# Kernel optimization log

Hardware: AMD Instinct MI355X
Metric: run time of the kernel (lower is better)

## Reference

```python
import jax, jax.numpy as jnp
import numpy as np

HEADS = 8
C_HEAD = 64  # head dim == in_dim of x
P0, P1 = 2, 3  # adaptive pool output


def setup_inputs() -> dict:
    key = jax.random.key(0)
    ks = jax.random.split(key, 8)
    b, c, h, w = 16, 64, 64, 96
    m, d = 6, 192
    inner = HEADS * C_HEAD  # 512
    return {
        "x": jax.random.normal(ks[0], (b, c, h, w), dtype=jnp.float32),
        "z": jax.random.normal(ks[1], (b, m, d), dtype=jnp.float32),
        "conv_w": jax.random.normal(ks[2], (192, c), dtype=jnp.float32) * 0.02,
        "conv_b": jax.random.normal(ks[3], (192,), dtype=jnp.float32) * 0.02,
        "wq": jax.random.normal(ks[4], (d, inner), dtype=jnp.float32) * 0.02,
        "bq": jax.random.normal(ks[5], (inner,), dtype=jnp.float32) * 0.02,
        "wo": jax.random.normal(ks[6], (inner, d), dtype=jnp.float32) * 0.02,
        "bo": jax.random.normal(ks[7], (d,), dtype=jnp.float32) * 0.02,
    }


def reference(x, z, conv_w, conv_b, wq, bq, wo, bo):
    b, c, h, w = x.shape
    _, m, d = z.shape
    # 1x1 conv (pointwise GEMM over channels) + bias
    xp = jnp.einsum('bchw,oc->bohw', x, conv_w) + conv_b[None, :, None, None]
    # AdaptiveAvgPool2d((2,3)) with exact divisibility -> block mean
    xp = xp.reshape(b, 192, P0, h // P0, P1, w // P1).mean(axis=(3, 5))  # [b,192,2,3]
    # view(b, d, m) then permute(0,2,1) -> [b, m, d]
    z = z + xp.reshape(b, d, m).transpose(0, 2, 1)
    # k = v: view(b, h*w, c), repeat heads along last dim, view(b, heads, h*w, c)
    # (row-major reshape reproduces torch .view semantics exactly)
    kv = jnp.tile(x.reshape(b, h * w, c), (1, 1, HEADS)).reshape(b, HEADS, h * w, C_HEAD)
    # q = Linear(dim, heads*c) then view(b, heads, m, c)
    q = (z @ wq + bq).reshape(b, HEADS, m, C_HEAD)
    scale = C_HEAD ** -0.5
    dots = jnp.einsum('bhmc,bhlc->bhml', q, kv) * scale  # [b,h,m,l]
    attn = jax.nn.softmax(dots, axis=-1)
    out = jnp.einsum('bhml,bhlc->bhmc', attn, kv)
    out = out.transpose(0, 2, 1, 3).reshape(b, m, HEADS * C_HEAD)  # b m (h c)
    return z + out @ wo + bo
```

## Files before the change

kernel.cpp:

```cpp
#include <hip/hip_runtime.h>

#define NB 16
#define NC 64
#define NM 6
#define ND 192
#define NHEADS 8
#define NCH 64
#define NINNER 512
#define PLANE 6144
#define XB (NC*PLANE)
#define NKEY 768
#define NCHUNK 8
#define CK 96

__global__ __launch_bounds__(256) void pool_kernel(const float* __restrict__ x,
                                                   float* __restrict__ xmean) {
    int bc = blockIdx.x;
    const float4* p = (const float4*)(x + (size_t)bc * PLANE);
    int tid = threadIdx.x;
    float acc[6] = {0.f,0.f,0.f,0.f,0.f,0.f};
    #pragma unroll
    for (int k = 0; k < 6; ++k) {
        int idx4 = tid + k * 256;
        int hh = idx4 / 24;
        int w4 = idx4 - hh * 24;
        int j = (hh >> 5) * 3 + (w4 >> 3);
        float4 v = p[idx4];
        acc[j] += v.x + v.y + v.z + v.w;
    }
    int lane = tid & 63, wave = tid >> 6;
    #pragma unroll
    for (int j = 0; j < 6; ++j) {
        float v = acc[j];
        for (int off = 32; off > 0; off >>= 1) v += __shfl_down(v, off, 64);
        acc[j] = v;
    }
    __shared__ float part[4][6];
    if (lane == 0) {
        #pragma unroll
        for (int j = 0; j < 6; ++j) part[wave][j] = acc[j];
    }
    __syncthreads();
    if (tid < 6) {
        float s = part[0][tid] + part[1][tid] + part[2][tid] + part[3][tid];
        xmean[bc * 6 + tid] = s * (1.0f / 1024.0f);
    }
}

__global__ __launch_bounds__(256) void zq_kernel(const float* __restrict__ z,
                                                 const float* __restrict__ conv_w,
                                                 const float* __restrict__ conv_b,
                                                 const float* __restrict__ wq,
                                                 const float* __restrict__ bq,
                                                 const float* __restrict__ xmean,
                                                 float* __restrict__ znew,
                                                 float* __restrict__ qr) {
    int blk = blockIdx.x;
    int cgrp = blk & 7, bm = blk >> 3;
    int b = bm / NM, m = bm - b * NM;
    int tid = threadIdx.x;
    __shared__ float xm[NC];
    __shared__ float zn[ND];
    __shared__ float qpart[3][64];
    if (tid < NC) xm[tid] = xmean[(b * NC + tid) * NM + m];
    __syncthreads();
    if (tid < ND) {
        float a = conv_b[tid];
        const float* wr = conv_w + tid * NC;
        #pragma unroll 16
        for (int c = 0; c < NC; ++c) a += wr[c] * xm[c];
        float v = z[bm * ND + tid] + a;
        zn[tid] = v;
        if (cgrp == 0) znew[bm * ND + tid] = v;
    }
    __syncthreads();
    int colL = tid & 63, ks = tid >> 6;
    int col = cgrp * 64 + colL;
    float a = (ks == 0) ? bq[col] : 0.f;
    int d0 = ks * 48;
    #pragma unroll 8
    for (int d = d0; d < d0 + 48; ++d) a += zn[d] * wq[d * NINNER + col];
    if (ks > 0) qpart[ks - 1][colL] = a;
    __syncthreads();
    if (ks == 0) {
        float tot = a + qpart[0][colL] + qpart[1][colL] + qpart[2][colL];
        int t = m * 8 + cgrp;
        qr[b * (48 * 64) + t * 64 + colL] = tot;
    }
}

__global__ __launch_bounds__(256, 4) void fattn_kernel(const float* __restrict__ x,
                                                       const float* __restrict__ qr,
                                                       float* __restrict__ po,
                                                       float* __restrict__ ps) {
    int blk = blockIdx.x;
    int chunk = blk & 7, bh = blk >> 3;
    int head = bh & 7, b = bh >> 3;
    int tid = threadIdx.x;
    __shared__ float k_lds[CK][NCH + 1];
    __shared__ float q_lds[NM][NCH];
    __shared__ float s_lds[NM][CK];
    __shared__ float pvp[3][NM][NCH];
    __shared__ float den_lds[NM];
    const float* kbase = x + (size_t)b * XB + (size_t)(head * NKEY + chunk * CK) * NCH;

    for (int i = tid; i < NM * NCH; i += 256) {
        int mi = i >> 6, ch = i & 63;
        q_lds[mi][ch] = qr[b * (48 * 64) + (head * NM + mi) * 64 + ch];
    }
    const float4* k4 = (const float4*)kbase;
    for (int i = tid; i < CK * 16; i += 256) {
        int row = i >> 4, c4 = i & 15;
        float4 v = k4[i];
        k_lds[row][c4 * 4 + 0] = v.x;
        k_lds[row][c4 * 4 + 1] = v.y;
        k_lds[row][c4 * 4 + 2] = v.z;
        k_lds[row][c4 * 4 + 3] = v.w;
    }
    __syncthreads();

    if (tid < 192) {
        int mip = (tid & 1) * 3, u = tid >> 1;
        float a0 = 0.f, a1 = 0.f, a2 = 0.f;
        #pragma unroll
        for (int c = 0; c < NCH; ++c) {
            float kv = k_lds[u][c];
            a0 += kv * q_lds[mip + 0][c];
            a1 += kv * q_lds[mip + 1][c];
            a2 += kv * q_lds[mip + 2][c];
        }
        s_lds[mip + 0][u] = __expf(a0 * 0.125f);
        s_lds[mip + 1][u] = __expf(a1 * 0.125f);
        s_lds[mip + 2][u] = __expf(a2 * 0.125f);
    }
    __syncthreads();

    int lane = tid & 63, wave = tid >> 6;
    #pragma unroll
    for (int rb = 0; rb < 2; ++rb) {
        int mi = rb * 4 + wave;
        if (mi < NM) {
            float v = s_lds[mi][lane] + ((lane < 32) ? s_lds[mi][64 + lane] : 0.f);
            for (int msk = 1; msk < 64; msk <<= 1) v += __shfl_xor(v, msk, 64);
            if (lane == 0) den_lds[mi] = v;
        }
    }

    float acc[NM] = {0.f,0.f,0.f,0.f,0.f,0.f};
    {
        int uq = tid >> 6, ch = tid & 63;
        int u0 = uq * 24;
        #pragma unroll 8
        for (int uu = u0; uu < u0 + 24; ++uu) {
            float kv = k_lds[uu][ch];
            #pragma unroll
            for (int mo = 0; mo < NM; ++mo) acc[mo] += s_lds[mo][uu] * kv;
        }
        if (uq > 0) {
            #pragma unroll
            for (int mo = 0; mo < NM; ++mo) pvp[uq - 1][mo][ch] = acc[mo];
        }
    }
    __syncthreads();
    if (tid < 64) {
        int ch = tid;
        #pragma unroll
        for (int mo = 0; mo < NM; ++mo) {
            float o = acc[mo] + pvp[0][mo][ch] + pvp[1][mo][ch] + pvp[2][mo][ch];
            po[(size_t)blk * (NM * NCH) + mo * NCH + ch] = o;
        }
    } else if (tid < 64 + NM) {
        ps[blk * NM + (tid - 64)] = den_lds[tid - 64];
    }
}

__global__ __launch_bounds__(256) void proj_kernel(const float* __restrict__ znew,
                                                   const float* __restrict__ po,
                                                   const float* __restrict__ ps,
                                                   const float* __restrict__ wo,
                                                   const float* __restrict__ bo,
                                                   float* __restrict__ out) {
    int blk = blockIdx.x;
    int cgrp = blk & 3, bm = blk >> 2;
    int b = bm / NM, m = bm - b * NM;
    int tid = threadIdx.x;
    __shared__ float orow[NINNER];
    __shared__ float part[3][48];

    for (int i = tid; i < NINNER; i += 256) {
        int h = i >> 6, ch = i & 63;
        int base = (b * NHEADS + h) * NCHUNK;
        float num = 0.f, den = 0.f;
        #pragma unroll
        for (int c = 0; c < NCHUNK; ++c) {
            num += po[(size_t)(base + c) * (NM * NCH) + m * NCH + ch];
            den += ps[(base + c) * NM + m];
        }
        orow[i] = num / den;
    }
    __syncthreads();

    int ks = tid / 48;
    int colL = tid - ks * 48;
    float a = 0.f;
    int col = cgrp * 48 + ((tid < 192) ? colL : 0);
    if (tid < 192) {
        int i0 = ks * 128;
        #pragma unroll 8
        for (int i = i0; i < i0 + 128; ++i) a += orow[i] * wo[i * ND + col];
        if (ks > 0) part[ks - 1][colL] = a;
    }
    __syncthreads();
    if (tid < 48) {
        float tot = a + part[0][colL] + part[1][colL] + part[2][colL]
                  + bo[col] + znew[bm * ND + col];
        out[bm * ND + col] = tot;
    }
}

extern "C" void kernel_launch(void* const* d_in, const int* in_sizes, int n_in,
                              void* d_out, int out_size, void* d_ws, size_t ws_size,
                              hipStream_t stream) {
    const float* x      = (const float*)d_in[0];
    const float* z      = (const float*)d_in[1];
    const float* conv_w = (const float*)d_in[2];
    const float* conv_b = (const float*)d_in[3];
    const float* wq     = (const float*)d_in[4];
    const float* bq     = (const float*)d_in[5];
    const float* wo     = (const float*)d_in[6];
    const float* bo     = (const float*)d_in[7];
    float* out = (float*)d_out;

    float* ws    = (float*)d_ws;
    float* xmean = ws;
    float* znew  = ws + 6144;
    float* qr    = ws + 24576;
    float* po    = ws + 73728;
    float* ps    = ws + 466944;

    pool_kernel<<<NB*NC, 256, 0, stream>>>(x, xmean);
    zq_kernel<<<NB*NM*8, 256, 0, stream>>>(z, conv_w, conv_b, wq, bq, xmean, znew, qr);
    fattn_kernel<<<NB*NHEADS*NCHUNK, 256, 0, stream>>>(x, qr, po, ps);
    proj_kernel<<<NB*NM*4, 256, 0, stream>>>(znew, po, ps, wo, bo, out);
}
```

Baseline: 37.04 us.

## Fuse z-update and q projection into attention kernel, prefetch K into registers

Removes the separate zq kernel by having each attention block recompute the updated z rows for its batch and the q vectors for its head, then run the chunked attention. K tiles are loaded into registers before the q computation to overlap global loads with that work, and shared memory is reused through a scratch buffer. This removes one launch and the qr workspace round trip, at the cost of heavily redundant per-block recomputation of z and q.

```diff
diff --git a/kernel.cpp b/kernel.cpp
--- a/kernel.cpp
+++ b/kernel.cpp
@@ -8,8 +8,6 @@
 #define NCH 64
 #define NINNER 512
 #define PLANE 6144
-#define XB (NC*PLANE)
-#define NKEY 768
 #define NCHUNK 8
 #define CK 96
 
@@ -47,91 +45,88 @@
     }
 }
 
-__global__ __launch_bounds__(256) void zq_kernel(const float* __restrict__ z,
-                                                 const float* __restrict__ conv_w,
-                                                 const float* __restrict__ conv_b,
-                                                 const float* __restrict__ wq,
-                                                 const float* __restrict__ bq,
-                                                 const float* __restrict__ xmean,
-                                                 float* __restrict__ znew,
-                                                 float* __restrict__ qr) {
+__global__ __launch_bounds__(256, 4) void qattn_kernel(
+    const float* __restrict__ x, const float* __restrict__ z,
+    const float* __restrict__ conv_w, const float* __restrict__ conv_b,
+    const float* __restrict__ wq, const float* __restrict__ bq,
+    const float* __restrict__ xmean,
+    float* __restrict__ znew, float* __restrict__ po, float* __restrict__ ps)
+{
     int blk = blockIdx.x;
-    int cgrp = blk & 7, bm = blk >> 3;
-    int b = bm / NM, m = bm - b * NM;
+    int b = blk >> 6, c = blk & 63;
+    int head = c >> 3;
     int tid = threadIdx.x;
-    __shared__ float xm[NC];
-    __shared__ float zn[ND];
-    __shared__ float qpart[3][64];
-    if (tid < NC) xm[tid] = xmean[(b * NC + tid) * NM + m];
-    __syncthreads();
-    if (tid < ND) {
-        float a = conv_b[tid];
-        const float* wr = conv_w + tid * NC;
-        #pragma unroll 16
-        for (int c = 0; c < NC; ++c) a += wr[c] * xm[c];
-        float v = z[bm * ND + tid] + a;
-        zn[tid] = v;
-        if (cgrp == 0) znew[bm * ND + tid] = v;
-    }
-    __syncthreads();
-    int colL = tid & 63, ks = tid >> 6;
-    int col = cgrp * 64 + colL;
-    float a = (ks == 0) ? bq[col] : 0.f;
-    int d0 = ks * 48;
-    #pragma unroll 8
-    for (int d = d0; d < d0 + 48; ++d) a += zn[d] * wq[d * NINNER + col];
-    if (ks > 0) qpart[ks - 1][colL] = a;
-    __syncthreads();
-    if (ks == 0) {
-        float tot = a + qpart[0][colL] + qpart[1][colL] + qpart[2][colL];
-        int t = m * 8 + cgrp;
-        qr[b * (48 * 64) + t * 64 + colL] = tot;
-    }
-}
-
-__global__ __launch_bounds__(256, 4) void fattn_kernel(const float* __restrict__ x,
-                                                       const float* __restrict__ qr,
-                                                       float* __restrict__ po,
-                                                       float* __restrict__ ps) {
-    int blk = blockIdx.x;
-    int chunk = blk & 7, bh = blk >> 3;
-    int head = bh & 7, b = bh >> 3;
-    int tid = threadIdx.x;
+
     __shared__ float k_lds[CK][NCH + 1];
     __shared__ float q_lds[NM][NCH];
-    __shared__ float s_lds[NM][CK];
-    __shared__ float pvp[3][NM][NCH];
-    __shared__ float den_lds[NM];
-    const float* kbase = x + (size_t)b * XB + (size_t)(head * NKEY + chunk * CK) * NCH;
-
-    for (int i = tid; i < NM * NCH; i += 256) {
-        int mi = i >> 6, ch = i & 63;
-        q_lds[mi][ch] = qr[b * (48 * 64) + (head * NM + mi) * 64 + ch];
-    }
-    const float4* k4 = (const float4*)kbase;
-    for (int i = tid; i < CK * 16; i += 256) {
-        int row = i >> 4, c4 = i & 15;
-        float4 v = k4[i];
-        k_lds[row][c4 * 4 + 0] = v.x;
-        k_lds[row][c4 * 4 + 1] = v.y;
-        k_lds[row][c4 * 4 + 2] = v.z;
-        k_lds[row][c4 * 4 + 3] = v.w;
-    }
-    __syncthreads();
+    __shared__ float scratch[1740];
+
+    float4 kreg[6];
+    {
+        const float4* k4 = (const float4*)(x + (size_t)blk * PLANE);
+        #pragma unroll
+        for (int r = 0; r < 6; ++r) kreg[r] = k4[tid + r * 256];
+    }
+
+    float* zn_s = scratch;
+    float* xm_s = scratch + 1152;
+    for (int i = tid; i < NC * NM; i += 256) xm_s[i] = xmean[b * (NC * NM) + i];
+    __syncthreads();
+
+    for (int i = tid; i < NM * ND; i += 256) {
+        int m = i / ND, d = i - m * ND;
+        float a = conv_b[d];
+        const float* wr = conv_w + d * NC;
+        #pragma unroll 16
+        for (int cc = 0; cc < NC; ++cc) a += wr[cc] * xm_s[cc * NM + m];
+        a += z[b * (NM * ND) + i];
+        zn_s[i] = a;
+        if (c == 0) znew[b * (NM * ND) + i] = a;
+    }
+    __syncthreads();
+
+    {
+        for (int idx = tid; idx < NM * NCH; idx += 256) {
+            int mi = idx >> 6, ch = idx & 63;
+            int flat = head * (NM * NCH) + idx;
+            int mrow = flat >> 9;
+            int col  = flat & 511;
+            float a = bq[col];
+            const float* zr = zn_s + mrow * ND;
+            #pragma unroll 8
+            for (int d = 0; d < ND; ++d) a += zr[d] * wq[d * NINNER + col];
+            q_lds[mi][ch] = a;
+        }
+    }
+
+    #pragma unroll
+    for (int r = 0; r < 6; ++r) {
+        int idx4 = tid + r * 256;
+        int u = idx4 >> 4, c4 = idx4 & 15;
+        k_lds[u][c4 * 4 + 0] = kreg[r].x;
+        k_lds[u][c4 * 4 + 1] = kreg[r].y;
+        k_lds[u][c4 * 4 + 2] = kreg[r].z;
+        k_lds[u][c4 * 4 + 3] = kreg[r].w;
+    }
+    __syncthreads();
+
+    float* s_s   = scratch;
+    float* pvp   = scratch + 576;
+    float* den_s = scratch + 1728;
 
     if (tid < 192) {
         int mip = (tid & 1) * 3, u = tid >> 1;
         float a0 = 0.f, a1 = 0.f, a2 = 0.f;
         #pragma unroll
-        for (int c = 0; c < NCH; ++c) {
-            float kv = k_lds[u][c];
-            a0 += kv * q_lds[mip + 0][c];
-            a1 += kv * q_lds[mip + 1][c];
-            a2 += kv * q_lds[mip + 2][c];
-        }
-        s_lds[mip + 0][u] = __expf(a0 * 0.125f);
-        s_lds[mip + 1][u] = __expf(a1 * 0.125f);
-        s_lds[mip + 2][u] = __expf(a2 * 0.125f);
+        for (int cc = 0; cc < NCH; ++cc) {
+            float kv = k_lds[u][cc];
+            a0 += kv * q_lds[mip + 0][cc];
+            a1 += kv * q_lds[mip + 1][cc];
+            a2 += kv * q_lds[mip + 2][cc];
+        }
+        s_s[(mip + 0) * CK + u] = __expf(a0 * 0.125f);
+        s_s[(mip + 1) * CK + u] = __expf(a1 * 0.125f);
+        s_s[(mip + 2) * CK + u] = __expf(a2 * 0.125f);
     }
     __syncthreads();
 
@@ -140,9 +135,9 @@
     for (int rb = 0; rb < 2; ++rb) {
         int mi = rb * 4 + wave;
         if (mi < NM) {
-            float v = s_lds[mi][lane] + ((lane < 32) ? s_lds[mi][64 + lane] : 0.f);
+            float v = s_s[mi * CK + lane] + ((lane < 32) ? s_s[mi * CK + 64 + lane] : 0.f);
             for (int msk = 1; msk < 64; msk <<= 1) v += __shfl_xor(v, msk, 64);
-            if (lane == 0) den_lds[mi] = v;
+            if (lane == 0) den_s[mi] = v;
         }
     }
 
@@ -154,11 +149,11 @@
         for (int uu = u0; uu < u0 + 24; ++uu) {
             float kv = k_lds[uu][ch];
             #pragma unroll
-            for (int mo = 0; mo < NM; ++mo) acc[mo] += s_lds[mo][uu] * kv;
+            for (int mo = 0; mo < NM; ++mo) acc[mo] += s_s[mo * CK + uu] * kv;
         }
         if (uq > 0) {
             #pragma unroll
-            for (int mo = 0; mo < NM; ++mo) pvp[uq - 1][mo][ch] = acc[mo];
+            for (int mo = 0; mo < NM; ++mo) pvp[((uq - 1) * NM + mo) * NCH + ch] = acc[mo];
         }
     }
     __syncthreads();
@@ -166,11 +161,13 @@
         int ch = tid;
         #pragma unroll
         for (int mo = 0; mo < NM; ++mo) {
-            float o = acc[mo] + pvp[0][mo][ch] + pvp[1][mo][ch] + pvp[2][mo][ch];
+            float o = acc[mo] + pvp[(0 * NM + mo) * NCH + ch]
+                              + pvp[(1 * NM + mo) * NCH + ch]
+                              + pvp[(2 * NM + mo) * NCH + ch];
             po[(size_t)blk * (NM * NCH) + mo * NCH + ch] = o;
         }
     } else if (tid < 64 + NM) {
-        ps[blk * NM + (tid - 64)] = den_lds[tid - 64];
+        ps[blk * NM + (tid - 64)] = den_s[tid - 64];
     }
 }
 
@@ -192,9 +189,9 @@
         int base = (b * NHEADS + h) * NCHUNK;
         float num = 0.f, den = 0.f;
         #pragma unroll
-        for (int c = 0; c < NCHUNK; ++c) {
-            num += po[(size_t)(base + c) * (NM * NCH) + m * NCH + ch];
-            den += ps[(base + c) * NM + m];
+        for (int cu = 0; cu < NCHUNK; ++cu) {
+            num += po[(size_t)(base + cu) * (NM * NCH) + m * NCH + ch];
+            den += ps[(base + cu) * NM + m];
         }
         orow[i] = num / den;
     }
@@ -234,12 +231,11 @@
     float* ws    = (float*)d_ws;
     float* xmean = ws;
     float* znew  = ws + 6144;
-    float* qr    = ws + 24576;
-    float* po    = ws + 73728;
-    float* ps    = ws + 466944;
+    float* po    = ws + 24576;
+    float* ps    = ws + 417792;
 
     pool_kernel<<<NB*NC, 256, 0, stream>>>(x, xmean);
-    zq_kernel<<<NB*NM*8, 256, 0, stream>>>(z, conv_w, conv_b, wq, bq, xmean, znew, qr);
-    fattn_kernel<<<NB*NHEADS*NCHUNK, 256, 0, stream>>>(x, qr, po, ps);
+    qattn_kernel<<<NB*NC, 256, 0, stream>>>(x, z, conv_w, conv_b, wq, bq,
+                                            xmean, znew, po, ps);
     proj_kernel<<<NB*NM*4, 256, 0, stream>>>(znew, po, ps, wo, bo, out);
 }
```

Measured after the change: 69.73 us. 1.88x slower.

## Split attention into 16 smaller key segments with vectorized LDS and shuffle reductions

Applied to the files above, without the earlier changes.

The attention kernel now handles 48 keys per block instead of 96, doubling the grid to 2048 blocks and raising the launch-bounds occupancy hint. K rows are padded to 68 floats so they can be stored and read as float4, and the QK dot products use float4 loads. The PV partial sums are combined with cross-lane shuffles instead of an LDS scratch buffer plus a barrier, and denominators are written straight to global memory. In exchange, the projection kernel has to combine twice as many partial results, and the workspace offset for the denominators moves.

```diff
diff --git a/kernel.cpp b/kernel.cpp
--- a/kernel.cpp
+++ b/kernel.cpp
@@ -10,8 +10,9 @@
 #define PLANE 6144
 #define XB (NC*PLANE)
 #define NKEY 768
-#define NCHUNK 8
-#define CK 96
+#define NSEG 16
+#define HC 48
+#define KP 68
 
 __global__ __launch_bounds__(256) void pool_kernel(const float* __restrict__ x,
                                                    float* __restrict__ xmean) {
@@ -89,45 +90,45 @@
     }
 }
 
-__global__ __launch_bounds__(256, 4) void fattn_kernel(const float* __restrict__ x,
+__global__ __launch_bounds__(256, 8) void fattn_kernel(const float* __restrict__ x,
                                                        const float* __restrict__ qr,
                                                        float* __restrict__ po,
                                                        float* __restrict__ ps) {
     int blk = blockIdx.x;
-    int chunk = blk & 7, bh = blk >> 3;
+    int seg = blk & 15, bh = blk >> 4;
     int head = bh & 7, b = bh >> 3;
     int tid = threadIdx.x;
-    __shared__ float k_lds[CK][NCH + 1];
+    __shared__ float k_lds[HC][KP];
     __shared__ float q_lds[NM][NCH];
-    __shared__ float s_lds[NM][CK];
-    __shared__ float pvp[3][NM][NCH];
-    __shared__ float den_lds[NM];
-    const float* kbase = x + (size_t)b * XB + (size_t)(head * NKEY + chunk * CK) * NCH;
+    __shared__ float s_lds[NM][52];
+    const float* kbase = x + (size_t)b * XB + (size_t)(head * NKEY + seg * HC) * NCH;
 
     for (int i = tid; i < NM * NCH; i += 256) {
         int mi = i >> 6, ch = i & 63;
         q_lds[mi][ch] = qr[b * (48 * 64) + (head * NM + mi) * 64 + ch];
     }
     const float4* k4 = (const float4*)kbase;
-    for (int i = tid; i < CK * 16; i += 256) {
+    #pragma unroll
+    for (int r = 0; r < 3; ++r) {
+        int i = tid + r * 256;
         int row = i >> 4, c4 = i & 15;
         float4 v = k4[i];
-        k_lds[row][c4 * 4 + 0] = v.x;
-        k_lds[row][c4 * 4 + 1] = v.y;
-        k_lds[row][c4 * 4 + 2] = v.z;
-        k_lds[row][c4 * 4 + 3] = v.w;
-    }
-    __syncthreads();
-
-    if (tid < 192) {
-        int mip = (tid & 1) * 3, u = tid >> 1;
+        *(float4*)&k_lds[row][c4 * 4] = v;
+    }
+    __syncthreads();
+
+    if (tid < 96) {
+        int u = tid >> 1, mip = (tid & 1) * 3;
         float a0 = 0.f, a1 = 0.f, a2 = 0.f;
         #pragma unroll
-        for (int c = 0; c < NCH; ++c) {
-            float kv = k_lds[u][c];
-            a0 += kv * q_lds[mip + 0][c];
-            a1 += kv * q_lds[mip + 1][c];
-            a2 += kv * q_lds[mip + 2][c];
+        for (int c = 0; c < 16; ++c) {
+            float4 kv = *(const float4*)&k_lds[u][c * 4];
+            float4 q0 = *(const float4*)&q_lds[mip + 0][c * 4];
+            float4 q1 = *(const float4*)&q_lds[mip + 1][c * 4];
+            float4 q2 = *(const float4*)&q_lds[mip + 2][c * 4];
+            a0 += kv.x*q0.x + kv.y*q0.y + kv.z*q0.z + kv.w*q0.w;
+            a1 += kv.x*q1.x + kv.y*q1.y + kv.z*q1.z + kv.w*q1.w;
+            a2 += kv.x*q2.x + kv.y*q2.y + kv.z*q2.z + kv.w*q2.w;
         }
         s_lds[mip + 0][u] = __expf(a0 * 0.125f);
         s_lds[mip + 1][u] = __expf(a1 * 0.125f);
@@ -136,41 +137,35 @@
     __syncthreads();
 
     int lane = tid & 63, wave = tid >> 6;
+
     #pragma unroll
     for (int rb = 0; rb < 2; ++rb) {
         int mi = rb * 4 + wave;
         if (mi < NM) {
-            float v = s_lds[mi][lane] + ((lane < 32) ? s_lds[mi][64 + lane] : 0.f);
+            float v = (lane < HC) ? s_lds[mi][lane] : 0.f;
             for (int msk = 1; msk < 64; msk <<= 1) v += __shfl_xor(v, msk, 64);
-            if (lane == 0) den_lds[mi] = v;
-        }
-    }
-
-    float acc[NM] = {0.f,0.f,0.f,0.f,0.f,0.f};
+            if (lane == 0) ps[blk * NM + mi] = v;
+        }
+    }
+
     {
-        int uq = tid >> 6, ch = tid & 63;
-        int u0 = uq * 24;
-        #pragma unroll 8
-        for (int uu = u0; uu < u0 + 24; ++uu) {
-            float kv = k_lds[uu][ch];
+        int chL = lane & 15, rg = lane >> 4;
+        int ch = wave * 16 + chL;
+        float acc[NM] = {0.f,0.f,0.f,0.f,0.f,0.f};
+        #pragma unroll
+        for (int i = 0; i < 12; ++i) {
+            int u = rg + i * 4;
+            float kv = k_lds[u][ch];
             #pragma unroll
-            for (int mo = 0; mo < NM; ++mo) acc[mo] += s_lds[mo][uu] * kv;
-        }
-        if (uq > 0) {
-            #pragma unroll
-            for (int mo = 0; mo < NM; ++mo) pvp[uq - 1][mo][ch] = acc[mo];
-        }
-    }
-    __syncthreads();
-    if (tid < 64) {
-        int ch = tid;
+            for (int mo = 0; mo < NM; ++mo) acc[mo] += s_lds[mo][u] * kv;
+        }
         #pragma unroll
         for (int mo = 0; mo < NM; ++mo) {
-            float o = acc[mo] + pvp[0][mo][ch] + pvp[1][mo][ch] + pvp[2][mo][ch];
-            po[(size_t)blk * (NM * NCH) + mo * NCH + ch] = o;
-        }
-    } else if (tid < 64 + NM) {
-        ps[blk * NM + (tid - 64)] = den_lds[tid - 64];
+            float v = acc[mo];
+            v += __shfl_xor(v, 16, 64);
+            v += __shfl_xor(v, 32, 64);
+            if (rg == 0) po[(size_t)blk * (NM * NCH) + mo * NCH + ch] = v;
+        }
     }
 }
 
@@ -189,12 +184,12 @@
 
     for (int i = tid; i < NINNER; i += 256) {
         int h = i >> 6, ch = i & 63;
-        int base = (b * NHEADS + h) * NCHUNK;
+        int base = (b * NHEADS + h) * NSEG;
         float num = 0.f, den = 0.f;
         #pragma unroll
-        for (int c = 0; c < NCHUNK; ++c) {
-            num += po[(size_t)(base + c) * (NM * NCH) + m * NCH + ch];
-            den += ps[(base + c) * NM + m];
+        for (int cu = 0; cu < NSEG; ++cu) {
+            num += po[(size_t)(base + cu) * (NM * NCH) + m * NCH + ch];
+            den += ps[(base + cu) * NM + m];
         }
         orow[i] = num / den;
     }
@@ -236,10 +231,10 @@
     float* znew  = ws + 6144;
     float* qr    = ws + 24576;
     float* po    = ws + 73728;
-    float* ps    = ws + 466944;
+    float* ps    = ws + 860160;
 
     pool_kernel<<<NB*NC, 256, 0, stream>>>(x, xmean);
     zq_kernel<<<NB*NM*8, 256, 0, stream>>>(z, conv_w, conv_b, wq, bq, xmean, znew, qr);
-    fattn_kernel<<<NB*NHEADS*NCHUNK, 256, 0, stream>>>(x, qr, po, ps);
+    fattn_kernel<<<NB*NHEADS*NSEG, 256, 0, stream>>>(x, qr, po, ps);
     proj_kernel<<<NB*NM*4, 256, 0, stream>>>(znew, po, ps, wo, bo, out);
 }
```

Measured after the change: 47.21 us. 27.4% more time.

## Vectorize LDS accesses and register-block QK scores in attention kernel

Applied to the files above, without the earlier changes.

The attention kernel now pads K and Q rows to 68 floats so it can write and read LDS with float4. The QK score stage uses 48 threads, each computing a 4x3 register tile with float4 loads. The PV stage reads scores as float4 across four keys at a time. The softmax denominator is written straight to global memory instead of through LDS. This cuts LDS instruction count and bank traffic, but leaves only 48 threads doing the score stage, so that stage may serialize and hurt latency.

```diff
diff --git a/kernel.cpp b/kernel.cpp
--- a/kernel.cpp
+++ b/kernel.cpp
@@ -12,6 +12,8 @@
 #define NKEY 768
 #define NCHUNK 8
 #define CK 96
+#define KP 68
+#define SP 100
 
 __global__ __launch_bounds__(256) void pool_kernel(const float* __restrict__ x,
                                                    float* __restrict__ xmean) {
@@ -97,11 +99,10 @@
     int chunk = blk & 7, bh = blk >> 3;
     int head = bh & 7, b = bh >> 3;
     int tid = threadIdx.x;
-    __shared__ float k_lds[CK][NCH + 1];
-    __shared__ float q_lds[NM][NCH];
-    __shared__ float s_lds[NM][CK];
+    __shared__ float k_lds[CK][KP];
+    __shared__ float q_lds[NM][KP];
+    __shared__ float s_lds[NM][SP];
     __shared__ float pvp[3][NM][NCH];
-    __shared__ float den_lds[NM];
     const float* kbase = x + (size_t)b * XB + (size_t)(head * NKEY + chunk * CK) * NCH;
 
     for (int i = tid; i < NM * NCH; i += 256) {
@@ -109,40 +110,51 @@
         q_lds[mi][ch] = qr[b * (48 * 64) + (head * NM + mi) * 64 + ch];
     }
     const float4* k4 = (const float4*)kbase;
-    for (int i = tid; i < CK * 16; i += 256) {
+    #pragma unroll
+    for (int r = 0; r < 6; ++r) {
+        int i = tid + r * 256;
         int row = i >> 4, c4 = i & 15;
         float4 v = k4[i];
-        k_lds[row][c4 * 4 + 0] = v.x;
-        k_lds[row][c4 * 4 + 1] = v.y;
-        k_lds[row][c4 * 4 + 2] = v.z;
-        k_lds[row][c4 * 4 + 3] = v.w;
-    }
-    __syncthreads();
-
-    if (tid < 192) {
-        int mip = (tid & 1) * 3, u = tid >> 1;
-        float a0 = 0.f, a1 = 0.f, a2 = 0.f;
-        #pragma unroll
-        for (int c = 0; c < NCH; ++c) {
-            float kv = k_lds[u][c];
-            a0 += kv * q_lds[mip + 0][c];
-            a1 += kv * q_lds[mip + 1][c];
-            a2 += kv * q_lds[mip + 2][c];
-        }
-        s_lds[mip + 0][u] = __expf(a0 * 0.125f);
-        s_lds[mip + 1][u] = __expf(a1 * 0.125f);
-        s_lds[mip + 2][u] = __expf(a2 * 0.125f);
+        *(float4*)&k_lds[row][c4 * 4] = v;
+    }
+    __syncthreads();
+
+    if (tid < 48) {
+        int t = tid >> 1, mip = (tid & 1) * 3;
+        float a[4][3];
+        #pragma unroll
+        for (int j = 0; j < 4; ++j) { a[j][0] = 0.f; a[j][1] = 0.f; a[j][2] = 0.f; }
+        #pragma unroll 4
+        for (int c = 0; c < 16; ++c) {
+            float4 q0 = *(const float4*)&q_lds[mip + 0][c * 4];
+            float4 q1 = *(const float4*)&q_lds[mip + 1][c * 4];
+            float4 q2 = *(const float4*)&q_lds[mip + 2][c * 4];
+            #pragma unroll
+            for (int j = 0; j < 4; ++j) {
+                float4 kv = *(const float4*)&k_lds[t + 24 * j][c * 4];
+                a[j][0] += kv.x*q0.x + kv.y*q0.y + kv.z*q0.z + kv.w*q0.w;
+                a[j][1] += kv.x*q1.x + kv.y*q1.y + kv.z*q1.z + kv.w*q1.w;
+                a[j][2] += kv.x*q2.x + kv.y*q2.y + kv.z*q2.z + kv.w*q2.w;
+            }
+        }
+        #pragma unroll
+        for (int j = 0; j < 4; ++j) {
+            s_lds[mip + 0][t + 24 * j] = __expf(a[j][0] * 0.125f);
+            s_lds[mip + 1][t + 24 * j] = __expf(a[j][1] * 0.125f);
+            s_lds[mip + 2][t + 24 * j] = __expf(a[j][2] * 0.125f);
+        }
     }
     __syncthreads();
 
     int lane = tid & 63, wave = tid >> 6;
+
     #pragma unroll
     for (int rb = 0; rb < 2; ++rb) {
         int mi = rb * 4 + wave;
         if (mi < NM) {
             float v = s_lds[mi][lane] + ((lane < 32) ? s_lds[mi][64 + lane] : 0.f);
             for (int msk = 1; msk < 64; msk <<= 1) v += __shfl_xor(v, msk, 64);
-            if (lane == 0) den_lds[mi] = v;
+            if (lane == 0) ps[blk * NM + mi] = v;
         }
     }
 
@@ -150,11 +162,24 @@
     {
         int uq = tid >> 6, ch = tid & 63;
         int u0 = uq * 24;
-        #pragma unroll 8
-        for (int uu = u0; uu < u0 + 24; ++uu) {
-            float kv = k_lds[uu][ch];
-            #pragma unroll
-            for (int mo = 0; mo < NM; ++mo) acc[mo] += s_lds[mo][uu] * kv;
+        #pragma unroll
+        for (int ub = 0; ub < 6; ++ub) {
+            float4 s0 = *(const float4*)&s_lds[0][u0 + ub * 4];
+            float4 s1 = *(const float4*)&s_lds[1][u0 + ub * 4];
+            float4 s2 = *(const float4*)&s_lds[2][u0 + ub * 4];
+            float4 s3 = *(const float4*)&s_lds[3][u0 + ub * 4];
+            float4 s4 = *(const float4*)&s_lds[4][u0 + ub * 4];
+            float4 s5 = *(const float4*)&s_lds[5][u0 + ub * 4];
+            float kv0 = k_lds[u0 + ub * 4 + 0][ch];
+            float kv1 = k_lds[u0 + ub * 4 + 1][ch];
+            float kv2 = k_lds[u0 + ub * 4 + 2][ch];
+            float kv3 = k_lds[u0 + ub * 4 + 3][ch];
+            acc[0] += s0.x*kv0 + s0.y*kv1 + s0.z*kv2 + s0.w*kv3;
+            acc[1] += s1.x*kv0 + s1.y*kv1 + s1.z*kv2 + s1.w*kv3;
+            acc[2] += s2.x*kv0 + s2.y*kv1 + s2.z*kv2 + s2.w*kv3;
+            acc[3] += s3.x*kv0 + s3.y*kv1 + s3.z*kv2 + s3.w*kv3;
+            acc[4] += s4.x*kv0 + s4.y*kv1 + s4.z*kv2 + s4.w*kv3;
+            acc[5] += s5.x*kv0 + s5.y*kv1 + s5.z*kv2 + s5.w*kv3;
         }
         if (uq > 0) {
             #pragma unroll
@@ -169,8 +194,6 @@
             float o = acc[mo] + pvp[0][mo][ch] + pvp[1][mo][ch] + pvp[2][mo][ch];
             po[(size_t)blk * (NM * NCH) + mo * NCH + ch] = o;
         }
-    } else if (tid < 64 + NM) {
-        ps[blk * NM + (tid - 64)] = den_lds[tid - 64];
     }
 }
 
```

Result: no change. 36.73 us (-0.9%).
